# Kernel optimization log

Hardware: AMD Instinct MI355X
Metric: run time of the kernel (lower is better)

Reference implementation:

```python
import jax, jax.numpy as jnp
import numpy as np
import math

WS = (8, 8)        # window_size for context (2D)
HEADS = 8


def _attend(q, k, v, h):
    # q: (Bw, Nq, inner), k/v: (Bw, Nk, inner)
    Bw, Nq, inner = q.shape
    d = inner // h
    q = q.reshape(Bw, Nq, h, d)
    k = k.reshape(Bw, -1, h, d)
    v = v.reshape(Bw, -1, h, d)
    scores = jnp.einsum('bqhd,bkhd->bhqk', q, k) * (d ** -0.5)
    attn = jax.nn.softmax(scores, axis=-1)
    out = jnp.einsum('bhqk,bkhd->bqhd', attn, v)
    return out.reshape(Bw, Nq, inner)


def reference(x, context, W_q, W_k, W_v, W_out, b_out):
    B, C, T, H, W = x.shape
    H_, W_ = context.shape[-2], context.shape[-1]
    ws = WS
    assert H_ * W_ > ws[0] * ws[1] and H * W >= ws[0] * ws[1]  # window branch
    # pad context to multiple of window_size (no-op for chosen shapes)
    pad_r_2d = (-W_) % ws[1]
    pad_b_2d = (-H_) % ws[0]
    context = jnp.pad(context, ((0, 0), (0, 0), (0, pad_b_2d), (0, pad_r_2d)))
    # scaled window size for the (smaller) 3D query tensor
    ws_ = (math.ceil(float(ws[0]) * H / H_), math.ceil(float(ws[1]) * W / W_))
    pad_r_3d = (-W) % ws_[1]
    pad_b_3d = (-H) % ws_[0]
    x = jnp.pad(x, ((0, 0), (0, 0), (0, 0), (0, pad_b_3d), (0, pad_r_3d)))
    Hp, Wp = x.shape[-2], x.shape[-1]
    Hc, Wc = context.shape[-2], context.shape[-1]
    # window partition: context (B,C,Hc,Wc) -> (B*h*w, ws0*ws1, C)
    hc, wc = Hc // ws[0], Wc // ws[1]
    ctx = context.reshape(B, C, hc, ws[0], wc, ws[1])
    ctx = ctx.transpose(0, 2, 4, 3, 5, 1).reshape(B * hc * wc, ws[0] * ws[1], C)
    # window partition: x (B,C,T,Hp,Wp) -> (B*h*w, T*ws_0*ws_1, C)
    hg, wg = Hp // ws_[0], Wp // ws_[1]
    xw = x.reshape(B, C, T, hg, ws_[0], wg, ws_[1])
    xw = xw.transpose(0, 3, 5, 2, 4, 6, 1).reshape(B * hg * wg, T * ws_[0] * ws_[1], C)
    # QKV projections (no bias: qkv_bias=False, to_k always bias-free)
    q = xw @ W_q
    k = ctx @ W_k
    v = ctx @ W_v
    out = _attend(q, k, v, HEADS)  # (Bw, Nq, inner)
    inner = out.shape[-1]
    # window reverse -> (B, inner, T, Hp, Wp)
    out = out.reshape(B, hg, wg, T, ws_[0], ws_[1], inner)
    out = out.transpose(0, 6, 3, 1, 4, 2, 5).reshape(B, inner, T, Hp, Wp)
    out = out[:, :, :, :H, :W]
    # b c t h w -> b (t h w) c
    out = out.transpose(0, 2, 3, 4, 1).reshape(B, T * H * W, inner)
    return out @ W_out + b_out


def setup_inputs() -> dict:
    key = jax.random.key(0)
    ks = jax.random.split(key, 7)
    D = 512
    s = 0.02
    return {
        'x': jax.random.normal(ks[0], (4, D, 4, 32, 32), jnp.float32),
        'context': jax.random.normal(ks[1], (4, D, 128, 128), jnp.float32),
        'W_q': jax.random.normal(ks[2], (D, D), jnp.float32) * s,
        'W_k': jax.random.normal(ks[3], (D, D), jnp.float32) * s,
        'W_v': jax.random.normal(ks[4], (D, D), jnp.float32) * s,
        'W_out': jax.random.normal(ks[5], (D, D), jnp.float32) * s,
        'b_out': jnp.zeros((D,), jnp.float32),
    }
```

## Files before the change

kernel.cpp:

```cpp
#include <hip/hip_runtime.h>
#include <hip/hip_bf16.h>

typedef unsigned short u16;
typedef unsigned int u32;
typedef unsigned long long u64;
typedef __attribute__((ext_vector_type(4))) float f32x4;
typedef __attribute__((ext_vector_type(4))) u16 u16x4;
typedef __attribute__((ext_vector_type(8))) u16 u16x8;
typedef __attribute__((ext_vector_type(8))) short s16x8;

__device__ __forceinline__ u16 f2bf(float f) {
    union { float f; u32 u; } v; v.f = f;
    u32 r = v.u + 0x7FFFu + ((v.u >> 16) & 1u);
    return (u16)(r >> 16);
}

__device__ __forceinline__ void gl_lds16(const u16* g, u16* l) {
    __builtin_amdgcn_global_load_lds(
        (const __attribute__((address_space(1))) unsigned int*)(const void*)g,
        (__attribute__((address_space(3))) unsigned int*)(void*)l, 16, 0, 0);
}

__global__ __launch_bounds__(256) void prep_kernel(
    const float* __restrict__ w0, const float* __restrict__ w1,
    const float* __restrict__ w2, const float* __restrict__ w3, u16* __restrict__ WT,
    const float* __restrict__ x, u16* __restrict__ Aq,
    const float* __restrict__ ctx, u16* __restrict__ Actx) {
    __shared__ char smem[16640];
    int bid = blockIdx.x;
    int tid = threadIdx.x;
    if (bid < 8192) {
        u16 (*t)[68] = (u16(*)[68])smem;
        int b2 = bid;
        int cb = b2 & 7; b2 >>= 3;
        int xb = b2 & 1; b2 >>= 1;
        int y  = b2 & 127; b2 >>= 7;
        int b  = b2;
        long ibase = ((long)(b * 512 + cb * 64) * 128 + y) * 128 + xb * 64;
#pragma unroll
        for (int p = 0; p < 4; ++p) {
            int task = p * 256 + tid;
            int cc = task >> 4, xl = (task & 15) * 4;
            float4 v = *(const float4*)&ctx[ibase + (long)cc * 16384 + xl];
            u16x4 o = {f2bf(v.x), f2bf(v.y), f2bf(v.z), f2bf(v.w)};
            *(u16x4*)&t[cc][xl] = o;
        }
        __syncthreads();
#pragma unroll
        for (int p = 0; p < 2; ++p) {
            int task = p * 256 + tid;
            int xx = task >> 3, j = task & 7;
            u16x8 o;
#pragma unroll
            for (int i = 0; i < 8; ++i) o[i] = t[j * 8 + i][xx];
            int xg = xb * 64 + xx;
            int row = b * 16384 + (y >> 3) * 1024 + (xg >> 3) * 64 + (y & 7) * 8 + (xg & 7);
            *(u16x8*)&Actx[(long)row * 512 + cb * 64 + j * 8] = o;
        }
    } else if (bid < 12288) {
        u16 (*t)[36] = (u16(*)[36])smem;
        int b2 = bid - 8192;
        int cb = b2 & 7; b2 >>= 3;
        int y  = b2 & 31; b2 >>= 5;
        int tt = b2 & 3; b2 >>= 2;
        int b  = b2;
        long ibase = ((long)(b * 512 + cb * 64) * 4 + tt) * 1024 + y * 32;
#pragma unroll
        for (int p = 0; p < 2; ++p) {
            int task = p * 256 + tid;
            int cc = task >> 3, xl = (task & 7) * 4;
            float4 v = *(const float4*)&x[ibase + (long)cc * 4096 + xl];
            u16x4 o = {f2bf(v.x), f2bf(v.y), f2bf(v.z), f2bf(v.w)};
            *(u16x4*)&t[cc][xl] = o;
        }
        __syncthreads();
        {
            int xx = tid >> 3, j = tid & 7;
            u16x8 o;
#pragma unroll
            for (int i = 0; i < 8; ++i) o[i] = t[j * 8 + i][xx];
            int row = b * 4096 + (y >> 1) * 256 + (xx >> 1) * 16 + tt * 4 + (y & 1) * 2 + (xx & 1);
            *(u16x8*)&Aq[(long)row * 512 + cb * 64 + j * 8] = o;
        }
    } else {
        float (*t)[65] = (float(*)[65])smem;
        int b2 = bid - 12288;
        int wsel = b2 >> 6;
        int tile = b2 & 63;
        int j0 = (tile >> 3) * 64, c0 = (tile & 7) * 64;
        const float* src = wsel == 0 ? w0 : wsel == 1 ? w1 : wsel == 2 ? w2 : w3;
        u16* out = WT + (long)wsel * 512 * 512;
        int tj = tid & 63;
        int ti = tid >> 6;
#pragma unroll
        for (int p = 0; p < 16; ++p) {
            int row = p * 4 + ti;
            t[row][tj] = src[(long)(c0 + row) * 512 + j0 + tj];
        }
        __syncthreads();
#pragma unroll
        for (int p = 0; p < 16; ++p) {
            int jl = p * 4 + ti;
            out[(long)(j0 + jl) * 512 + c0 + tj] = f2bf(t[tj][jl]);
        }
    }
}

template <int FINAL>
__global__ __launch_bounds__(256, 4) void gemm128_kernel(
    const u16* __restrict__ A, const u16* __restrict__ Bt,
    u16* __restrict__ Cb, float* __restrict__ Cf, const float* __restrict__ bias) {
    __shared__ u16 As[1024 * 8];
    __shared__ u16 Bs[1024 * 8];
    int tid = threadIdx.x;
    int lane = tid & 63;
    int w = tid >> 6;
    int wm = w >> 1, wn = w & 1;
    int bid = blockIdx.x;
    int wg = (bid & 7) * 64 + (bid >> 3);
    int m0 = (wg >> 2) * 128;
    int n0 = (wg & 3) * 128;

    const f32x4 z = {0.f, 0.f, 0.f, 0.f};
    f32x4 acc[4][4];
#pragma unroll
    for (int i = 0; i < 4; ++i)
#pragma unroll
        for (int j = 0; j < 4; ++j) acc[i][j] = z;

    int aoff[4], boff[4], lb[4];
#pragma unroll
    for (int i = 0; i < 4; ++i) {
        int s = i * 256 + tid;
        int row = s >> 3;
        int cb = (s & 7) ^ (row & 7);
        aoff[i] = (m0 + row) * 512 + cb * 8;
        boff[i] = (n0 + row) * 512 + cb * 8;
        lb[i] = (i * 256 + w * 64) * 8;
    }
    int la = lane & 15, lg = lane >> 4;
    for (int ks = 0; ks < 8; ++ks) {
        int ko = ks * 64;
#pragma unroll
        for (int i = 0; i < 4; ++i) {
            gl_lds16(&A[aoff[i] + ko], &As[lb[i]]);
            gl_lds16(&Bt[boff[i] + ko], &Bs[lb[i]]);
        }
        __syncthreads();
#pragma unroll
        for (int kk = 0; kk < 2; ++kk) {
            int cb = kk * 4 + lg;
            s16x8 af[4], bfr[4];
#pragma unroll
            for (int mt = 0; mt < 4; ++mt) {
                int r = wm * 64 + mt * 16 + la;
                af[mt] = *(const s16x8*)&As[r * 64 + ((cb ^ (r & 7)) * 8)];
            }
#pragma unroll
            for (int nt = 0; nt < 4; ++nt) {
                int c = wn * 64 + nt * 16 + la;
                bfr[nt] = *(const s16x8*)&Bs[c * 64 + ((cb ^ (c & 7)) * 8)];
            }
#pragma unroll
            for (int mt = 0; mt < 4; ++mt)
#pragma unroll
                for (int nt = 0; nt < 4; ++nt)
                    acc[mt][nt] = __builtin_amdgcn_mfma_f32_16x16x32_bf16(af[mt], bfr[nt], acc[mt][nt], 0, 0, 0);
        }
        __syncthreads();
    }
#pragma unroll
    for (int mt = 0; mt < 4; ++mt) {
#pragma unroll
        for (int nt = 0; nt < 4; ++nt) {
            int col = n0 + wn * 64 + nt * 16 + la;
#pragma unroll
            for (int rr = 0; rr < 4; ++rr) {
                int r = m0 + wm * 64 + mt * 16 + lg * 4 + rr;
                float v = acc[mt][nt][rr];
                if (FINAL) {
                    int bb = r >> 12, hg = (r >> 8) & 15, wgx = (r >> 4) & 15;
                    int tt = (r >> 2) & 3, rr0 = (r >> 1) & 1, cc0 = r & 1;
                    int tok = bb * 4096 + tt * 1024 + (hg * 2 + rr0) * 32 + wgx * 2 + cc0;
                    Cf[(long)tok * 512 + col] = v + bias[col];
                } else {
                    Cb[(long)r * 512 + col] = f2bf(v);
                }
            }
        }
    }
}

__global__ __launch_bounds__(512, 2) void gemmkv256_kernel(
    const u16* __restrict__ A, const u16* __restrict__ B,
    u16* __restrict__ CK, u16* __restrict__ CVT) {
    __shared__ u16 lds[2][2][16384];
    int tid = threadIdx.x;
    int lane = tid & 63;
    int w = tid >> 6;
    int wm = w >> 2, wn = w & 3;
    int la = lane & 15, lg = lane >> 4;
    int bid = blockIdx.x;
    int wg = (bid & 7) * 128 + (bid >> 3);
    int m0 = (wg >> 2) * 256;
    int n0 = (wg & 3) * 256;

    const f32x4 z = {0.f, 0.f, 0.f, 0.f};
    f32x4 acc[8][4];
#pragma unroll
    for (int i = 0; i < 8; ++i)
#pragma unroll
        for (int j = 0; j < 4; ++j) acc[i][j] = z;

    int aoff[4], boff[4], lsl[4];
#pragma unroll
    for (int i = 0; i < 4; ++i) {
        int s = i * 512 + tid;
        int row = s >> 3;
        int cb = (s & 7) ^ (row & 7);
        aoff[i] = (m0 + row) * 512 + cb * 8;
        boff[i] = (n0 + row) * 512 + cb * 8;
        lsl[i] = (i * 512 + w * 64) * 8;
    }

    s16x8 bfr[4][2];

#pragma unroll
    for (int i = 0; i < 4; ++i) {
        gl_lds16(&A[aoff[i]], &lds[0][0][lsl[i]]);
        gl_lds16(&B[boff[i]], &lds[0][1][lsl[i]]);
    }
#pragma unroll
    for (int i = 0; i < 4; ++i) {
        gl_lds16(&A[aoff[i] + 64], &lds[1][0][lsl[i]]);
        gl_lds16(&B[boff[i] + 64], &lds[1][1][lsl[i]]);
    }
    asm volatile("s_waitcnt vmcnt(8)" ::: "memory");
    __builtin_amdgcn_s_barrier();
    asm volatile("" ::: "memory");

#pragma unroll
    for (int t = 0; t < 8; ++t) {
        int buf = t & 1;
        const u16* Ab = lds[buf][0];
        const u16* Bb = lds[buf][1];
        int ko2 = (t + 2) * 64;

        {
            int cb = lg;
            s16x8 af[4];
#pragma unroll
            for (int mt = 0; mt < 4; ++mt) {
                int r = wm * 128 + mt * 16 + la;
                af[mt] = *(const s16x8*)&Ab[r * 64 + ((cb ^ (r & 7)) * 8)];
            }
#pragma unroll
            for (int nt = 0; nt < 4; ++nt) {
                int c = wn * 64 + nt * 16 + la;
                bfr[nt][0] = *(const s16x8*)&Bb[c * 64 + ((cb ^ (c & 7)) * 8)];
            }
            __builtin_amdgcn_s_barrier();
            __builtin_amdgcn_s_setprio(1);
#pragma unroll
            for (int mt = 0; mt < 4; ++mt)
#pragma unroll
                for (int nt = 0; nt < 4; ++nt)
                    acc[mt][nt] = __builtin_amdgcn_mfma_f32_16x16x32_bf16(af[mt], bfr[nt][0], acc[mt][nt], 0, 0, 0);
            __builtin_amdgcn_s_setprio(0);
            __builtin_amdgcn_sched_barrier(0);
            __builtin_amdgcn_s_barrier();
        }
        {
            int cb = 4 + lg;
            s16x8 af[4];
#pragma unroll
            for (int mt = 0; mt < 4; ++mt) {
                int r = wm * 128 + mt * 16 + la;
                af[mt] = *(const s16x8*)&Ab[r * 64 + ((cb ^ (r & 7)) * 8)];
            }
#pragma unroll
            for (int nt = 0; nt < 4; ++nt) {
                int c = wn * 64 + nt * 16 + la;
                bfr[nt][1] = *(const s16x8*)&Bb[c * 64 + ((cb ^ (c & 7)) * 8)];
            }
            __builtin_amdgcn_s_barrier();
            __builtin_amdgcn_s_setprio(1);
#pragma unroll
            for (int mt = 0; mt < 4; ++mt)
#pragma unroll
                for (int nt = 0; nt < 4; ++nt)
                    acc[mt][nt] = __builtin_amdgcn_mfma_f32_16x16x32_bf16(af[mt], bfr[nt][1], acc[mt][nt], 0, 0, 0);
            __builtin_amdgcn_s_setprio(0);
            __builtin_amdgcn_sched_barrier(0);
            __builtin_amdgcn_s_barrier();
        }
        {
            int cb = 4 + lg;
            s16x8 af[4];
#pragma unroll
            for (int mt = 0; mt < 4; ++mt) {
                int r = wm * 128 + 64 + mt * 16 + la;
                af[mt] = *(const s16x8*)&Ab[r * 64 + ((cb ^ (r & 7)) * 8)];
            }
            if (t < 6) {
                gl_lds16(&B[boff[0] + ko2], &lds[buf][1][lsl[0]]);
                gl_lds16(&B[boff[1] + ko2], &lds[buf][1][lsl[1]]);
                gl_lds16(&A[aoff[0] + ko2], &lds[buf][0][lsl[0]]);
            }
            __builtin_amdgcn_s_barrier();
            __builtin_amdgcn_s_setprio(1);
#pragma unroll
            for (int mt = 0; mt < 4; ++mt)
#pragma unroll
                for (int nt = 0; nt < 4; ++nt)
                    acc[4 + mt][nt] = __builtin_amdgcn_mfma_f32_16x16x32_bf16(af[mt], bfr[nt][1], acc[4 + mt][nt], 0, 0, 0);
            __builtin_amdgcn_s_setprio(0);
            __builtin_amdgcn_sched_barrier(0);
            __builtin_amdgcn_s_barrier();
        }
        {
            int cb = lg;
            s16x8 af[4];
#pragma unroll
            for (int mt = 0; mt < 4; ++mt) {
                int r = wm * 128 + 64 + mt * 16 + la;
                af[mt] = *(const s16x8*)&Ab[r * 64 + ((cb ^ (r & 7)) * 8)];
            }
            if (t < 6) {
                gl_lds16(&B[boff[2] + ko2], &lds[buf][1][lsl[2]]);
                gl_lds16(&B[boff[3] + ko2], &lds[buf][1][lsl[3]]);
                gl_lds16(&A[aoff[2] + ko2], &lds[buf][0][lsl[2]]);
            }
            __builtin_amdgcn_s_barrier();
            __builtin_amdgcn_s_setprio(1);
#pragma unroll
            for (int mt = 0; mt < 4; ++mt)
#pragma unroll
                for (int nt = 0; nt < 4; ++nt)
                    acc[4 + mt][nt] = __builtin_amdgcn_mfma_f32_16x16x32_bf16(af[mt], bfr[nt][0], acc[4 + mt][nt], 0, 0, 0);
            __builtin_amdgcn_s_setprio(0);
            __builtin_amdgcn_sched_barrier(0);
            __builtin_amdgcn_s_barrier();
        }
        if (t < 6) {
            gl_lds16(&A[aoff[1] + ko2], &lds[buf][0][lsl[1]]);
            gl_lds16(&A[aoff[3] + ko2], &lds[buf][0][lsl[3]]);
            asm volatile("s_waitcnt vmcnt(8)" ::: "memory");
            __builtin_amdgcn_s_barrier();
            asm volatile("" ::: "memory");
        } else if (t == 6) {
            asm volatile("s_waitcnt vmcnt(0)" ::: "memory");
            __builtin_amdgcn_s_barrier();
            asm volatile("" ::: "memory");
        }
    }

    if ((wg & 3) < 2) {
#pragma unroll
        for (int mt = 0; mt < 8; ++mt) {
#pragma unroll
            for (int nt = 0; nt < 4; ++nt) {
                int col = n0 + wn * 64 + nt * 16 + la;
#pragma unroll
                for (int rr = 0; rr < 4; ++rr) {
                    int r = m0 + wm * 128 + mt * 16 + lg * 4 + rr;
                    CK[(long)r * 512 + col] = f2bf(acc[mt][nt][rr]);
                }
            }
        }
    } else {
        u16* sl = ((u16*)lds) + w * 8192;
#pragma unroll
        for (int mt = 0; mt < 8; ++mt) {
            int winl = mt >> 2;
            int kv0 = (mt & 3) * 16 + lg * 4;
#pragma unroll
            for (int nt = 0; nt < 4; ++nt) {
                int dl = nt * 16 + la;
                int kvs = kv0 ^ ((dl & 7) << 3);
                u32 lo = (u32)f2bf(acc[mt][nt][0]) | ((u32)f2bf(acc[mt][nt][1]) << 16);
                u32 hi = (u32)f2bf(acc[mt][nt][2]) | ((u32)f2bf(acc[mt][nt][3]) << 16);
                u64 pk = (u64)lo | ((u64)hi << 32);
                *(u64*)&sl[winl * 4096 + dl * 64 + kvs] = pk;
            }
        }
        int winb = (m0 >> 6) + wm * 2;
        int dbase = (n0 - 512) + wn * 64;
#pragma unroll
        for (int it = 0; it < 16; ++it) {
            int g = it * 64 + lane;
            int winl = g >> 9;
            int rem = g & 511;
            int dl = rem >> 3;
            int kvg = rem & 7;
            u16x8 v = *(const u16x8*)&sl[winl * 4096 + dl * 64 + ((kvg * 8) ^ ((dl & 7) << 3))];
            *(u16x8*)&CVT[(long)(winb + winl) * 32768 + (dbase + dl) * 64 + kvg * 8] = v;
        }
    }
}

__global__ __launch_bounds__(256) void attn_kernel(
    const u16* __restrict__ Q, const u16* __restrict__ K,
    const u16* __restrict__ VT, u16* __restrict__ O) {
    __shared__ u16 P[4][16 * 104];
    int bid = blockIdx.x;
    int wgid = (bid & 7) * 256 + (bid >> 3);
    int tid = threadIdx.x;
    int wid = tid >> 6;
    int lane = tid & 63;
    int win = wgid >> 1;
    int h = (wgid & 1) * 4 + wid;
    int la = lane & 15, lg = lane >> 4;
    u16* Pw = P[wid];
    const u16* Qb = Q + (long)win * 16 * 512 + h * 64;
    const u16* Kb = K + (long)win * 64 * 512 + h * 64;
    const u16* Vt = VT + (long)win * 32768 + h * 64 * 64;

    s16x8 qf[2];
#pragma unroll
    for (int kk = 0; kk < 2; ++kk)
        qf[kk] = *(const s16x8*)&Qb[la * 512 + kk * 32 + lg * 8];

    const f32x4 z = {0.f, 0.f, 0.f, 0.f};
    f32x4 st[4];
#pragma unroll
    for (int rt = 0; rt < 4; ++rt) st[rt] = z;
#pragma unroll
    for (int rt = 0; rt < 4; ++rt)
#pragma unroll
        for (int kk = 0; kk < 2; ++kk) {
            s16x8 kf = *(const s16x8*)&Kb[(rt * 16 + la) * 512 + kk * 32 + lg * 8];
            st[rt] = __builtin_amdgcn_mfma_f32_16x16x32_bf16(kf, qf[kk], st[rt], 0, 0, 0);
        }
    float mloc = -1e30f;
#pragma unroll
    for (int rt = 0; rt < 4; ++rt)
#pragma unroll
        for (int rr = 0; rr < 4; ++rr) {
            st[rt][rr] *= 0.125f;
            mloc = fmaxf(mloc, st[rt][rr]);
        }
    mloc = fmaxf(mloc, __shfl_xor(mloc, 16));
    mloc = fmaxf(mloc, __shfl_xor(mloc, 32));
    float p[4][4];
    float sloc = 0.f;
#pragma unroll
    for (int rt = 0; rt < 4; ++rt)
#pragma unroll
        for (int rr = 0; rr < 4; ++rr) {
            p[rt][rr] = __expf(st[rt][rr] - mloc);
            sloc += p[rt][rr];
        }
    sloc += __shfl_xor(sloc, 16);
    sloc += __shfl_xor(sloc, 32);
    float inv = 1.0f / sloc;
#pragma unroll
    for (int rt = 0; rt < 4; ++rt)
#pragma unroll
        for (int rr = 0; rr < 4; ++rr)
            Pw[la * 104 + rt * 16 + lg * 4 + rr] = f2bf(p[rt][rr] * inv);
    __syncthreads();

    f32x4 od[4];
#pragma unroll
    for (int dt = 0; dt < 4; ++dt) od[dt] = z;
#pragma unroll
    for (int kk2 = 0; kk2 < 2; ++kk2) {
        s16x8 pa = *(const s16x8*)&Pw[la * 104 + kk2 * 32 + lg * 8];
#pragma unroll
        for (int dt = 0; dt < 4; ++dt) {
            s16x8 vb = *(const s16x8*)&Vt[(dt * 16 + la) * 64 + kk2 * 32 + lg * 8];
            od[dt] = __builtin_amdgcn_mfma_f32_16x16x32_bf16(pa, vb, od[dt], 0, 0, 0);
        }
    }
    u16* Ob = O + (long)win * 16 * 512 + h * 64;
#pragma unroll
    for (int dt = 0; dt < 4; ++dt)
#pragma unroll
        for (int rr = 0; rr < 4; ++rr)
            Ob[(long)(lg * 4 + rr) * 512 + dt * 16 + la] = f2bf(od[dt][rr]);
}

__global__ void sentinel_kernel(float* out) {
    if (threadIdx.x == 0 && blockIdx.x == 0) out[0] = -12345.0f;
}

extern "C" void kernel_launch(void* const* d_in, const int* in_sizes, int n_in,
                              void* d_out, int out_size, void* d_ws, size_t ws_size,
                              hipStream_t stream) {
    const float* x   = (const float*)d_in[0];
    const float* ctx = (const float*)d_in[1];
    const float* Wq  = (const float*)d_in[2];
    const float* Wk  = (const float*)d_in[3];
    const float* Wv  = (const float*)d_in[4];
    const float* Wo  = (const float*)d_in[5];
    const float* bo  = (const float*)d_in[6];
    float* out = (float*)d_out;

    u16* wsb  = (u16*)d_ws;
    u16* WT   = wsb;
    u16* Aq   = WT + 4l * 262144;
    u16* Actx = Aq + 8388608l;
    u16* Qb   = Actx + 33554432l;
    u16* Kb   = Qb + 8388608l;
    u16* VTb  = Kb + 33554432l;
    u16* Ob   = VTb + 33554432l;
    size_t need = (size_t)(126877696l) * 2;
    if (ws_size < need) {
        sentinel_kernel<<<1, 64, 0, stream>>>(out);
        return;
    }

    prep_kernel<<<12544, 256, 0, stream>>>(Wq, Wk, Wv, Wo, WT, x, Aq, ctx, Actx);
    gemm128_kernel<0><<<512, 256, 0, stream>>>(Aq, WT, Qb, nullptr, nullptr);
    gemmkv256_kernel<<<1024, 512, 0, stream>>>(Actx, WT + 262144l, Kb, VTb);
    attn_kernel<<<2048, 256, 0, stream>>>(Qb, Kb, VTb, Ob);
    gemm128_kernel<1><<<512, 256, 0, stream>>>(Ob, WT + 3l * 262144, nullptr, out, bo);
}
```

Baseline: 201.2 us.

## Make KV projection GEMM persistent and compute V transposed directly

Replaces the 1024-block KV GEMM with a 256-block persistent kernel in which each block loops over four 256-row M tiles. It prefetches the next tile's first K slices during the tail of the current tile, aiming to hide prologue load latency and cut launch and tail overhead. For V it swaps the operand roles (weights as A, context as B) so the output lands already transposed. This removes the LDS transpose staging, but the CVT stores become scalar, strided 2-byte writes.

```diff
diff --git a/kernel.cpp b/kernel.cpp
--- a/kernel.cpp
+++ b/kernel.cpp
@@ -3,7 +3,6 @@
 
 typedef unsigned short u16;
 typedef unsigned int u32;
-typedef unsigned long long u64;
 typedef __attribute__((ext_vector_type(4))) float f32x4;
 typedef __attribute__((ext_vector_type(4))) u16 u16x4;
 typedef __attribute__((ext_vector_type(8))) u16 u16x8;
@@ -191,8 +190,8 @@
     }
 }
 
-__global__ __launch_bounds__(512, 2) void gemmkv256_kernel(
-    const u16* __restrict__ A, const u16* __restrict__ B,
+__global__ __launch_bounds__(512, 2) void gemmkv_pers_kernel(
+    const u16* __restrict__ Actx, const u16* __restrict__ WTk, const u16* __restrict__ WTv,
     u16* __restrict__ CK, u16* __restrict__ CVT) {
     __shared__ u16 lds[2][2][16384];
     int tid = threadIdx.x;
@@ -201,9 +200,14 @@
     int wm = w >> 2, wn = w & 3;
     int la = lane & 15, lg = lane >> 4;
     int bid = blockIdx.x;
-    int wg = (bid & 7) * 128 + (bid >> 3);
-    int m0 = (wg >> 2) * 256;
-    int n0 = (wg & 3) * 256;
+    int wg = (bid & 7) * 32 + (bid >> 3);
+    int part = wg >> 7;
+    int u = wg & 127;
+    int mb = u >> 1;
+    int half = u & 1;
+
+    const u16* srcA = part ? WTv : Actx;
+    const u16* srcB = part ? Actx : WTk;
 
     const f32x4 z = {0.f, 0.f, 0.f, 0.f};
     f32x4 acc[8][4];
@@ -212,14 +216,16 @@
 #pragma unroll
         for (int j = 0; j < 4; ++j) acc[i][j] = z;
 
-    int aoff[4], boff[4], lsl[4];
+    int aC[4], bC[4], lsl[4];
 #pragma unroll
     for (int i = 0; i < 4; ++i) {
         int s = i * 512 + tid;
         int row = s >> 3;
         int cb = (s & 7) ^ (row & 7);
-        aoff[i] = (m0 + row) * 512 + cb * 8;
-        boff[i] = (n0 + row) * 512 + cb * 8;
+        int tok = (mb * 1024 + row) * 512 + cb * 8;
+        int wgt = (half * 256 + row) * 512 + cb * 8;
+        aC[i] = part ? wgt : tok;
+        bC[i] = part ? tok : wgt;
         lsl[i] = (i * 512 + w * 64) * 8;
     }
 
@@ -227,175 +233,193 @@
 
 #pragma unroll
     for (int i = 0; i < 4; ++i) {
-        gl_lds16(&A[aoff[i]], &lds[0][0][lsl[i]]);
-        gl_lds16(&B[boff[i]], &lds[0][1][lsl[i]]);
+        gl_lds16(&srcA[aC[i]], &lds[0][0][lsl[i]]);
+        gl_lds16(&srcB[bC[i]], &lds[0][1][lsl[i]]);
     }
 #pragma unroll
     for (int i = 0; i < 4; ++i) {
-        gl_lds16(&A[aoff[i] + 64], &lds[1][0][lsl[i]]);
-        gl_lds16(&B[boff[i] + 64], &lds[1][1][lsl[i]]);
+        gl_lds16(&srcA[aC[i] + 64], &lds[1][0][lsl[i]]);
+        gl_lds16(&srcB[bC[i] + 64], &lds[1][1][lsl[i]]);
     }
     asm volatile("s_waitcnt vmcnt(8)" ::: "memory");
     __builtin_amdgcn_s_barrier();
     asm volatile("" ::: "memory");
 
-#pragma unroll
-    for (int t = 0; t < 8; ++t) {
-        int buf = t & 1;
-        const u16* Ab = lds[buf][0];
-        const u16* Bb = lds[buf][1];
-        int ko2 = (t + 2) * 64;
-
-        {
-            int cb = lg;
-            s16x8 af[4];
-#pragma unroll
-            for (int mt = 0; mt < 4; ++mt) {
-                int r = wm * 128 + mt * 16 + la;
-                af[mt] = *(const s16x8*)&Ab[r * 64 + ((cb ^ (r & 7)) * 8)];
-            }
-#pragma unroll
-            for (int nt = 0; nt < 4; ++nt) {
-                int c = wn * 64 + nt * 16 + la;
-                bfr[nt][0] = *(const s16x8*)&Bb[c * 64 + ((cb ^ (c & 7)) * 8)];
-            }
-            __builtin_amdgcn_s_barrier();
-            __builtin_amdgcn_s_setprio(1);
-#pragma unroll
-            for (int mt = 0; mt < 4; ++mt)
-#pragma unroll
-                for (int nt = 0; nt < 4; ++nt)
-                    acc[mt][nt] = __builtin_amdgcn_mfma_f32_16x16x32_bf16(af[mt], bfr[nt][0], acc[mt][nt], 0, 0, 0);
-            __builtin_amdgcn_s_setprio(0);
-            __builtin_amdgcn_sched_barrier(0);
-            __builtin_amdgcn_s_barrier();
-        }
-        {
-            int cb = 4 + lg;
-            s16x8 af[4];
-#pragma unroll
-            for (int mt = 0; mt < 4; ++mt) {
-                int r = wm * 128 + mt * 16 + la;
-                af[mt] = *(const s16x8*)&Ab[r * 64 + ((cb ^ (r & 7)) * 8)];
-            }
-#pragma unroll
-            for (int nt = 0; nt < 4; ++nt) {
-                int c = wn * 64 + nt * 16 + la;
-                bfr[nt][1] = *(const s16x8*)&Bb[c * 64 + ((cb ^ (c & 7)) * 8)];
-            }
-            __builtin_amdgcn_s_barrier();
-            __builtin_amdgcn_s_setprio(1);
-#pragma unroll
-            for (int mt = 0; mt < 4; ++mt)
-#pragma unroll
-                for (int nt = 0; nt < 4; ++nt)
-                    acc[mt][nt] = __builtin_amdgcn_mfma_f32_16x16x32_bf16(af[mt], bfr[nt][1], acc[mt][nt], 0, 0, 0);
-            __builtin_amdgcn_s_setprio(0);
-            __builtin_amdgcn_sched_barrier(0);
-            __builtin_amdgcn_s_barrier();
-        }
-        {
-            int cb = 4 + lg;
-            s16x8 af[4];
-#pragma unroll
-            for (int mt = 0; mt < 4; ++mt) {
-                int r = wm * 128 + 64 + mt * 16 + la;
-                af[mt] = *(const s16x8*)&Ab[r * 64 + ((cb ^ (r & 7)) * 8)];
+#pragma unroll 1
+    for (int mt2 = 0; mt2 < 4; ++mt2) {
+        int aN[4], bN[4];
+#pragma unroll
+        for (int i = 0; i < 4; ++i) {
+            aN[i] = part ? aC[i] : aC[i] + 131072;
+            bN[i] = part ? bC[i] + 131072 : bC[i];
+        }
+        bool more = (mt2 < 3);
+
+#pragma unroll
+        for (int t = 0; t < 8; ++t) {
+            int buf = t & 1;
+            const u16* Ab = lds[buf][0];
+            const u16* Bb = lds[buf][1];
+            const int k2o = ((t + 2) & 7) * 64;
+
+            {
+                int cb = lg;
+                s16x8 af[4];
+#pragma unroll
+                for (int mt = 0; mt < 4; ++mt) {
+                    int r = wm * 128 + mt * 16 + la;
+                    af[mt] = *(const s16x8*)&Ab[r * 64 + ((cb ^ (r & 7)) * 8)];
+                }
+#pragma unroll
+                for (int nt = 0; nt < 4; ++nt) {
+                    int c = wn * 64 + nt * 16 + la;
+                    bfr[nt][0] = *(const s16x8*)&Bb[c * 64 + ((cb ^ (c & 7)) * 8)];
+                }
+                __builtin_amdgcn_s_barrier();
+                __builtin_amdgcn_s_setprio(1);
+#pragma unroll
+                for (int mt = 0; mt < 4; ++mt)
+#pragma unroll
+                    for (int nt = 0; nt < 4; ++nt)
+                        acc[mt][nt] = __builtin_amdgcn_mfma_f32_16x16x32_bf16(af[mt], bfr[nt][0], acc[mt][nt], 0, 0, 0);
+                __builtin_amdgcn_s_setprio(0);
+                __builtin_amdgcn_sched_barrier(0);
+                __builtin_amdgcn_s_barrier();
+            }
+            {
+                int cb = 4 + lg;
+                s16x8 af[4];
+#pragma unroll
+                for (int mt = 0; mt < 4; ++mt) {
+                    int r = wm * 128 + mt * 16 + la;
+                    af[mt] = *(const s16x8*)&Ab[r * 64 + ((cb ^ (r & 7)) * 8)];
+                }
+#pragma unroll
+                for (int nt = 0; nt < 4; ++nt) {
+                    int c = wn * 64 + nt * 16 + la;
+                    bfr[nt][1] = *(const s16x8*)&Bb[c * 64 + ((cb ^ (c & 7)) * 8)];
+                }
+                __builtin_amdgcn_s_barrier();
+                __builtin_amdgcn_s_setprio(1);
+#pragma unroll
+                for (int mt = 0; mt < 4; ++mt)
+#pragma unroll
+                    for (int nt = 0; nt < 4; ++nt)
+                        acc[mt][nt] = __builtin_amdgcn_mfma_f32_16x16x32_bf16(af[mt], bfr[nt][1], acc[mt][nt], 0, 0, 0);
+                __builtin_amdgcn_s_setprio(0);
+                __builtin_amdgcn_sched_barrier(0);
+                __builtin_amdgcn_s_barrier();
+            }
+            {
+                int cb = 4 + lg;
+                s16x8 af[4];
+#pragma unroll
+                for (int mt = 0; mt < 4; ++mt) {
+                    int r = wm * 128 + 64 + mt * 16 + la;
+                    af[mt] = *(const s16x8*)&Ab[r * 64 + ((cb ^ (r & 7)) * 8)];
+                }
+                if (t < 6) {
+                    gl_lds16(&srcB[bC[0] + k2o], &lds[buf][1][lsl[0]]);
+                    gl_lds16(&srcB[bC[1] + k2o], &lds[buf][1][lsl[1]]);
+                    gl_lds16(&srcA[aC[0] + k2o], &lds[buf][0][lsl[0]]);
+                } else if (more) {
+                    gl_lds16(&srcB[bN[0] + k2o], &lds[buf][1][lsl[0]]);
+                    gl_lds16(&srcB[bN[1] + k2o], &lds[buf][1][lsl[1]]);
+                    gl_lds16(&srcA[aN[0] + k2o], &lds[buf][0][lsl[0]]);
+                }
+                __builtin_amdgcn_s_barrier();
+                __builtin_amdgcn_s_setprio(1);
+#pragma unroll
+                for (int mt = 0; mt < 4; ++mt)
+#pragma unroll
+                    for (int nt = 0; nt < 4; ++nt)
+                        acc[4 + mt][nt] = __builtin_amdgcn_mfma_f32_16x16x32_bf16(af[mt], bfr[nt][1], acc[4 + mt][nt], 0, 0, 0);
+                __builtin_amdgcn_s_setprio(0);
+                __builtin_amdgcn_sched_barrier(0);
+                __builtin_amdgcn_s_barrier();
+            }
+            {
+                int cb = lg;
+                s16x8 af[4];
+#pragma unroll
+                for (int mt = 0; mt < 4; ++mt) {
+                    int r = wm * 128 + 64 + mt * 16 + la;
+                    af[mt] = *(const s16x8*)&Ab[r * 64 + ((cb ^ (r & 7)) * 8)];
+                }
+                if (t < 6) {
+                    gl_lds16(&srcB[bC[2] + k2o], &lds[buf][1][lsl[2]]);
+                    gl_lds16(&srcB[bC[3] + k2o], &lds[buf][1][lsl[3]]);
+                    gl_lds16(&srcA[aC[2] + k2o], &lds[buf][0][lsl[2]]);
+                } else if (more) {
+                    gl_lds16(&srcB[bN[2] + k2o], &lds[buf][1][lsl[2]]);
+                    gl_lds16(&srcB[bN[3] + k2o], &lds[buf][1][lsl[3]]);
+                    gl_lds16(&srcA[aN[2] + k2o], &lds[buf][0][lsl[2]]);
+                }
+                __builtin_amdgcn_s_barrier();
+                __builtin_amdgcn_s_setprio(1);
+#pragma unroll
+                for (int mt = 0; mt < 4; ++mt)
+#pragma unroll
+                    for (int nt = 0; nt < 4; ++nt)
+                        acc[4 + mt][nt] = __builtin_amdgcn_mfma_f32_16x16x32_bf16(af[mt], bfr[nt][0], acc[4 + mt][nt], 0, 0, 0);
+                __builtin_amdgcn_s_setprio(0);
+                __builtin_amdgcn_sched_barrier(0);
+                __builtin_amdgcn_s_barrier();
             }
             if (t < 6) {
-                gl_lds16(&B[boff[0] + ko2], &lds[buf][1][lsl[0]]);
-                gl_lds16(&B[boff[1] + ko2], &lds[buf][1][lsl[1]]);
-                gl_lds16(&A[aoff[0] + ko2], &lds[buf][0][lsl[0]]);
-            }
-            __builtin_amdgcn_s_barrier();
-            __builtin_amdgcn_s_setprio(1);
-#pragma unroll
-            for (int mt = 0; mt < 4; ++mt)
-#pragma unroll
-                for (int nt = 0; nt < 4; ++nt)
-                    acc[4 + mt][nt] = __builtin_amdgcn_mfma_f32_16x16x32_bf16(af[mt], bfr[nt][1], acc[4 + mt][nt], 0, 0, 0);
-            __builtin_amdgcn_s_setprio(0);
-            __builtin_amdgcn_sched_barrier(0);
-            __builtin_amdgcn_s_barrier();
-        }
-        {
-            int cb = lg;
-            s16x8 af[4];
-#pragma unroll
-            for (int mt = 0; mt < 4; ++mt) {
-                int r = wm * 128 + 64 + mt * 16 + la;
-                af[mt] = *(const s16x8*)&Ab[r * 64 + ((cb ^ (r & 7)) * 8)];
-            }
-            if (t < 6) {
-                gl_lds16(&B[boff[2] + ko2], &lds[buf][1][lsl[2]]);
-                gl_lds16(&B[boff[3] + ko2], &lds[buf][1][lsl[3]]);
-                gl_lds16(&A[aoff[2] + ko2], &lds[buf][0][lsl[2]]);
-            }
-            __builtin_amdgcn_s_barrier();
-            __builtin_amdgcn_s_setprio(1);
-#pragma unroll
-            for (int mt = 0; mt < 4; ++mt)
-#pragma unroll
-                for (int nt = 0; nt < 4; ++nt)
-                    acc[4 + mt][nt] = __builtin_amdgcn_mfma_f32_16x16x32_bf16(af[mt], bfr[nt][0], acc[4 + mt][nt], 0, 0, 0);
-            __builtin_amdgcn_s_setprio(0);
-            __builtin_amdgcn_sched_barrier(0);
-            __builtin_amdgcn_s_barrier();
-        }
-        if (t < 6) {
-            gl_lds16(&A[aoff[1] + ko2], &lds[buf][0][lsl[1]]);
-            gl_lds16(&A[aoff[3] + ko2], &lds[buf][0][lsl[3]]);
-            asm volatile("s_waitcnt vmcnt(8)" ::: "memory");
-            __builtin_amdgcn_s_barrier();
-            asm volatile("" ::: "memory");
-        } else if (t == 6) {
-            asm volatile("s_waitcnt vmcnt(0)" ::: "memory");
-            __builtin_amdgcn_s_barrier();
-            asm volatile("" ::: "memory");
-        }
-    }
-
-    if ((wg & 3) < 2) {
-#pragma unroll
-        for (int mt = 0; mt < 8; ++mt) {
-#pragma unroll
-            for (int nt = 0; nt < 4; ++nt) {
-                int col = n0 + wn * 64 + nt * 16 + la;
-#pragma unroll
-                for (int rr = 0; rr < 4; ++rr) {
-                    int r = m0 + wm * 128 + mt * 16 + lg * 4 + rr;
-                    CK[(long)r * 512 + col] = f2bf(acc[mt][nt][rr]);
-                }
-            }
-        }
-    } else {
-        u16* sl = ((u16*)lds) + w * 8192;
-#pragma unroll
-        for (int mt = 0; mt < 8; ++mt) {
-            int winl = mt >> 2;
-            int kv0 = (mt & 3) * 16 + lg * 4;
-#pragma unroll
-            for (int nt = 0; nt < 4; ++nt) {
-                int dl = nt * 16 + la;
-                int kvs = kv0 ^ ((dl & 7) << 3);
-                u32 lo = (u32)f2bf(acc[mt][nt][0]) | ((u32)f2bf(acc[mt][nt][1]) << 16);
-                u32 hi = (u32)f2bf(acc[mt][nt][2]) | ((u32)f2bf(acc[mt][nt][3]) << 16);
-                u64 pk = (u64)lo | ((u64)hi << 32);
-                *(u64*)&sl[winl * 4096 + dl * 64 + kvs] = pk;
-            }
-        }
-        int winb = (m0 >> 6) + wm * 2;
-        int dbase = (n0 - 512) + wn * 64;
-#pragma unroll
-        for (int it = 0; it < 16; ++it) {
-            int g = it * 64 + lane;
-            int winl = g >> 9;
-            int rem = g & 511;
-            int dl = rem >> 3;
-            int kvg = rem & 7;
-            u16x8 v = *(const u16x8*)&sl[winl * 4096 + dl * 64 + ((kvg * 8) ^ ((dl & 7) << 3))];
-            *(u16x8*)&CVT[(long)(winb + winl) * 32768 + (dbase + dl) * 64 + kvg * 8] = v;
-        }
+                gl_lds16(&srcA[aC[1] + k2o], &lds[buf][0][lsl[1]]);
+                gl_lds16(&srcA[aC[3] + k2o], &lds[buf][0][lsl[3]]);
+                asm volatile("s_waitcnt vmcnt(8)" ::: "memory");
+                __builtin_amdgcn_s_barrier();
+                asm volatile("" ::: "memory");
+            } else if (more) {
+                gl_lds16(&srcA[aN[1] + k2o], &lds[buf][0][lsl[1]]);
+                gl_lds16(&srcA[aN[3] + k2o], &lds[buf][0][lsl[3]]);
+                asm volatile("s_waitcnt vmcnt(8)" ::: "memory");
+                __builtin_amdgcn_s_barrier();
+                asm volatile("" ::: "memory");
+            } else if (t == 6) {
+                asm volatile("s_waitcnt vmcnt(0)" ::: "memory");
+                __builtin_amdgcn_s_barrier();
+                asm volatile("" ::: "memory");
+            }
+        }
+
+        int tokbase = mb * 1024 + mt2 * 256;
+        if (part == 0) {
+#pragma unroll
+            for (int mt = 0; mt < 8; ++mt) {
+#pragma unroll
+                for (int nt = 0; nt < 4; ++nt) {
+                    int col = half * 256 + wn * 64 + nt * 16 + la;
+#pragma unroll
+                    for (int rr = 0; rr < 4; ++rr) {
+                        int r = tokbase + wm * 128 + mt * 16 + lg * 4 + rr;
+                        CK[(long)r * 512 + col] = f2bf(acc[mt][nt][rr]);
+                    }
+                }
+            }
+        } else {
+            int winb = (tokbase >> 6) + wn;
+#pragma unroll
+            for (int mt = 0; mt < 8; ++mt) {
+#pragma unroll
+                for (int nt = 0; nt < 4; ++nt) {
+                    int kv = nt * 16 + la;
+#pragma unroll
+                    for (int rr = 0; rr < 4; ++rr) {
+                        int d = half * 256 + wm * 128 + mt * 16 + lg * 4 + rr;
+                        CVT[(long)winb * 32768 + d * 64 + kv] = f2bf(acc[mt][nt][rr]);
+                    }
+                }
+            }
+        }
+#pragma unroll
+        for (int i = 0; i < 8; ++i)
+#pragma unroll
+            for (int j = 0; j < 4; ++j) acc[i][j] = z;
+#pragma unroll
+        for (int i = 0; i < 4; ++i) { aC[i] = aN[i]; bC[i] = bN[i]; }
     }
 }
 
@@ -513,7 +537,7 @@
 
     prep_kernel<<<12544, 256, 0, stream>>>(Wq, Wk, Wv, Wo, WT, x, Aq, ctx, Actx);
     gemm128_kernel<0><<<512, 256, 0, stream>>>(Aq, WT, Qb, nullptr, nullptr);
-    gemmkv256_kernel<<<1024, 512, 0, stream>>>(Actx, WT + 262144l, Kb, VTb);
+    gemmkv_pers_kernel<<<256, 512, 0, stream>>>(Actx, WT + 262144l, WT + 2l * 262144, Kb, VTb);
     attn_kernel<<<2048, 256, 0, stream>>>(Qb, Kb, VTb, Ob);
     gemm128_kernel<1><<<512, 256, 0, stream>>>(Ob, WT + 3l * 262144, nullptr, out, bo);
 }
```

New measurement: 210.9 us. +4.8%, slower.

## Store K and V interleaved row-major and transpose V in attention LDS

Applied to the files above, without the earlier changes.

The KV GEMM epilogue no longer transposes V through LDS into a per-window V^T buffer. It writes K and V as one row-major [rows,1024] bf16 matrix. The attention kernel stages each head's V tile into padded LDS and gathers the transposed B-operand with scalar LDS reads. This moves transpose work from the GEMM epilogue to the attention kernel, adding LDS traffic and many 16-bit LDS reads per MFMA, and the strided V/K loads at 1024 stride may be less coalesced.

```diff
diff --git a/kernel.cpp b/kernel.cpp
--- a/kernel.cpp
+++ b/kernel.cpp
@@ -3,7 +3,6 @@
 
 typedef unsigned short u16;
 typedef unsigned int u32;
-typedef unsigned long long u64;
 typedef __attribute__((ext_vector_type(4))) float f32x4;
 typedef __attribute__((ext_vector_type(4))) u16 u16x4;
 typedef __attribute__((ext_vector_type(8))) u16 u16x8;
@@ -192,8 +191,7 @@
 }
 
 __global__ __launch_bounds__(512, 2) void gemmkv256_kernel(
-    const u16* __restrict__ A, const u16* __restrict__ B,
-    u16* __restrict__ CK, u16* __restrict__ CVT) {
+    const u16* __restrict__ A, const u16* __restrict__ B, u16* __restrict__ C) {
     __shared__ u16 lds[2][2][16384];
     int tid = threadIdx.x;
     int lane = tid & 63;
@@ -355,53 +353,23 @@
         }
     }
 
-    if ((wg & 3) < 2) {
-#pragma unroll
-        for (int mt = 0; mt < 8; ++mt) {
-#pragma unroll
-            for (int nt = 0; nt < 4; ++nt) {
-                int col = n0 + wn * 64 + nt * 16 + la;
-#pragma unroll
-                for (int rr = 0; rr < 4; ++rr) {
-                    int r = m0 + wm * 128 + mt * 16 + lg * 4 + rr;
-                    CK[(long)r * 512 + col] = f2bf(acc[mt][nt][rr]);
-                }
-            }
-        }
-    } else {
-        u16* sl = ((u16*)lds) + w * 8192;
-#pragma unroll
-        for (int mt = 0; mt < 8; ++mt) {
-            int winl = mt >> 2;
-            int kv0 = (mt & 3) * 16 + lg * 4;
-#pragma unroll
-            for (int nt = 0; nt < 4; ++nt) {
-                int dl = nt * 16 + la;
-                int kvs = kv0 ^ ((dl & 7) << 3);
-                u32 lo = (u32)f2bf(acc[mt][nt][0]) | ((u32)f2bf(acc[mt][nt][1]) << 16);
-                u32 hi = (u32)f2bf(acc[mt][nt][2]) | ((u32)f2bf(acc[mt][nt][3]) << 16);
-                u64 pk = (u64)lo | ((u64)hi << 32);
-                *(u64*)&sl[winl * 4096 + dl * 64 + kvs] = pk;
-            }
-        }
-        int winb = (m0 >> 6) + wm * 2;
-        int dbase = (n0 - 512) + wn * 64;
-#pragma unroll
-        for (int it = 0; it < 16; ++it) {
-            int g = it * 64 + lane;
-            int winl = g >> 9;
-            int rem = g & 511;
-            int dl = rem >> 3;
-            int kvg = rem & 7;
-            u16x8 v = *(const u16x8*)&sl[winl * 4096 + dl * 64 + ((kvg * 8) ^ ((dl & 7) << 3))];
-            *(u16x8*)&CVT[(long)(winb + winl) * 32768 + (dbase + dl) * 64 + kvg * 8] = v;
+#pragma unroll
+    for (int mt = 0; mt < 8; ++mt) {
+#pragma unroll
+        for (int nt = 0; nt < 4; ++nt) {
+            int col = n0 + wn * 64 + nt * 16 + la;
+#pragma unroll
+            for (int rr = 0; rr < 4; ++rr) {
+                int r = m0 + wm * 128 + mt * 16 + lg * 4 + rr;
+                C[(long)r * 1024 + col] = f2bf(acc[mt][nt][rr]);
+            }
         }
     }
 }
 
 __global__ __launch_bounds__(256) void attn_kernel(
-    const u16* __restrict__ Q, const u16* __restrict__ K,
-    const u16* __restrict__ VT, u16* __restrict__ O) {
+    const u16* __restrict__ Q, const u16* __restrict__ KV, u16* __restrict__ O) {
+    __shared__ u16 Vls[4][64][70];
     __shared__ u16 P[4][16 * 104];
     int bid = blockIdx.x;
     int wgid = (bid & 7) * 256 + (bid >> 3);
@@ -413,8 +381,19 @@
     int la = lane & 15, lg = lane >> 4;
     u16* Pw = P[wid];
     const u16* Qb = Q + (long)win * 16 * 512 + h * 64;
-    const u16* Kb = K + (long)win * 64 * 512 + h * 64;
-    const u16* Vt = VT + (long)win * 32768 + h * 64 * 64;
+    const u16* Kb = KV + (long)win * 64 * 1024 + h * 64;
+    const u16* Vb = KV + (long)win * 64 * 1024 + 512 + h * 64;
+
+    {
+        int rsel = lane >> 3;
+        int dsel = (lane & 7) * 8;
+#pragma unroll
+        for (int i = 0; i < 8; ++i) {
+            int kv = i * 8 + rsel;
+            s16x8 v = *(const s16x8*)&Vb[(long)kv * 1024 + dsel];
+            *(s16x8*)&Vls[wid][kv][dsel] = v;
+        }
+    }
 
     s16x8 qf[2];
 #pragma unroll
@@ -429,7 +408,7 @@
     for (int rt = 0; rt < 4; ++rt)
 #pragma unroll
         for (int kk = 0; kk < 2; ++kk) {
-            s16x8 kf = *(const s16x8*)&Kb[(rt * 16 + la) * 512 + kk * 32 + lg * 8];
+            s16x8 kf = *(const s16x8*)&Kb[(rt * 16 + la) * 1024 + kk * 32 + lg * 8];
             st[rt] = __builtin_amdgcn_mfma_f32_16x16x32_bf16(kf, qf[kk], st[rt], 0, 0, 0);
         }
     float mloc = -1e30f;
@@ -469,7 +448,10 @@
         s16x8 pa = *(const s16x8*)&Pw[la * 104 + kk2 * 32 + lg * 8];
 #pragma unroll
         for (int dt = 0; dt < 4; ++dt) {
-            s16x8 vb = *(const s16x8*)&Vt[(dt * 16 + la) * 64 + kk2 * 32 + lg * 8];
+            s16x8 vb;
+#pragma unroll
+            for (int j = 0; j < 8; ++j)
+                vb[j] = (short)Vls[wid][kk2 * 32 + lg * 8 + j][dt * 16 + la];
             od[dt] = __builtin_amdgcn_mfma_f32_16x16x32_bf16(pa, vb, od[dt], 0, 0, 0);
         }
     }
@@ -502,9 +484,8 @@
     u16* Aq   = WT + 4l * 262144;
     u16* Actx = Aq + 8388608l;
     u16* Qb   = Actx + 33554432l;
-    u16* Kb   = Qb + 8388608l;
-    u16* VTb  = Kb + 33554432l;
-    u16* Ob   = VTb + 33554432l;
+    u16* KVb  = Qb + 8388608l;
+    u16* Ob   = KVb + 67108864l;
     size_t need = (size_t)(126877696l) * 2;
     if (ws_size < need) {
         sentinel_kernel<<<1, 64, 0, stream>>>(out);
@@ -513,7 +494,7 @@
 
     prep_kernel<<<12544, 256, 0, stream>>>(Wq, Wk, Wv, Wo, WT, x, Aq, ctx, Actx);
     gemm128_kernel<0><<<512, 256, 0, stream>>>(Aq, WT, Qb, nullptr, nullptr);
-    gemmkv256_kernel<<<1024, 512, 0, stream>>>(Actx, WT + 262144l, Kb, VTb);
-    attn_kernel<<<2048, 256, 0, stream>>>(Qb, Kb, VTb, Ob);
+    gemmkv256_kernel<<<1024, 512, 0, stream>>>(Actx, WT + 262144l, KVb);
+    attn_kernel<<<2048, 256, 0, stream>>>(Qb, KVb, Ob);
     gemm128_kernel<1><<<512, 256, 0, stream>>>(Ob, WT + 3l * 262144, nullptr, out, bo);
 }
```

New measurement: 199.5 us. No clear change (-0.8%).
